# Optimization experiments

Measured on AMD Instinct MI355X. Metric: run time of the kernel, lower is better.

## Reference

```python
import jax, jax.numpy as jnp
import numpy as np

LOW_T = 25.5   # 0.1 * 255
HIGH_T = 76.5  # 0.3 * 255


def _dwconv3x3(img, k):
    # img: [B, C, H, W]; k: [3, 3]; depthwise conv with replicate border (as OpenCV Sobel)
    B, C, H, W = img.shape
    p = jnp.pad(img, ((0, 0), (0, 0), (1, 1), (1, 1)), mode='edge')
    kern = jnp.broadcast_to(k.astype(img.dtype), (C, 1, 3, 3))
    return jax.lax.conv_general_dilated(p, kern, (1, 1), 'VALID', feature_group_count=C)


def _shift(a, dy, dx):
    # a: [B, H, W]; shift by (dy, dx), zero at out-of-range borders
    B, H, W = a.shape
    p = jnp.pad(a, ((0, 0), (1, 1), (1, 1)))
    return p[:, 1 + dy:1 + dy + H, 1 + dx:1 + dx + W]


def canny(x, low, high):
    # x: [B, 3, H, W] in [0, 1]
    B, C, H, W = x.shape
    img = jnp.floor(jnp.clip(x, 0.0, 1.0) * 255.0)  # uint8 quantization, kept float

    kx = jnp.array([[-1., 0., 1.], [-2., 0., 2.], [-1., 0., 1.]])
    ky = jnp.array([[-1., -2., -1.], [0., 0., 0.], [1., 2., 1.]])
    gx = _dwconv3x3(img, kx)  # [B, C, H, W]
    gy = _dwconv3x3(img, ky)

    # L1 gradient magnitude (OpenCV default L2gradient=False); multi-channel:
    # pick the channel with max magnitude per pixel (OpenCV behavior)
    mag_c = jnp.abs(gx) + jnp.abs(gy)                      # [B, C, H, W]
    idx = jnp.argmax(mag_c, axis=1, keepdims=True)         # [B, 1, H, W]
    gxs = jnp.take_along_axis(gx, idx, axis=1)[:, 0]       # [B, H, W]
    gys = jnp.take_along_axis(gy, idx, axis=1)[:, 0]
    mag = jnp.take_along_axis(mag_c, idx, axis=1)[:, 0]

    # Non-maximum suppression: quantize gradient direction into 4 bins
    PI = np.float32(np.pi)
    ang = jnp.mod(jnp.arctan2(gys, gxs), PI)               # [0, pi)
    b = (jnp.floor((ang + PI / 8) / (PI / 4)).astype(jnp.int32)) % 4  # [B, H, W]

    # neighbor offsets along gradient direction per bin: 0deg, 45deg, 90deg, 135deg
    offs = [((0, 1), (0, -1)), ((1, 1), (-1, -1)), ((1, 0), (-1, 0)), ((1, -1), (-1, 1))]
    s1 = jnp.stack([_shift(mag, dy, dx) for (dy, dx), _ in offs])   # [4, B, H, W]
    s2 = jnp.stack([_shift(mag, dy, dx) for _, (dy, dx) in offs])
    n1 = jnp.take_along_axis(s1, b[None], axis=0)[0]
    n2 = jnp.take_along_axis(s2, b[None], axis=0)[0]
    nms = jnp.where((mag >= n1) & (mag >= n2), mag, 0.0)

    # Double threshold + hysteresis (8-connected propagation to fixed point)
    strong = (nms > high).astype(x.dtype)
    weak = (nms > low).astype(x.dtype)

    def cond(c):
        return c[1]

    def body(c):
        s, _ = c
        d = jax.lax.reduce_window(s, 0.0, jax.lax.max, (1, 3, 3), (1, 1, 1), 'SAME')
        ns = jnp.maximum(s, d * weak)
        return ns, jnp.any(ns != s)

    edges, _ = jax.lax.while_loop(cond, body, (strong, jnp.array(True)))

    # cv2.cvtColor GRAY2RGB then /255 -> {0, 1} replicated over 3 channels
    return jnp.broadcast_to(edges[:, None], (B, C, H, W))


def setup_inputs() -> dict:
    key = jax.random.key(0)
    x = jax.random.uniform(key, (16, 3, 720, 1280), dtype=jnp.float32)
    return {"x": x}


def reference(x):
    return canny(x, LOW_T, HIGH_T)
```

## Files before the change

### kernel.cpp

```cpp
#include <hip/hip_runtime.h>
#include <hip/hip_cooperative_groups.h>
#include <stdint.h>

namespace cg = cooperative_groups;
typedef unsigned long long u64;

static constexpr int BB  = 16;
static constexpr int HH  = 720;
static constexpr int WW  = 1280;
static constexpr int HWP = HH * WW;
static constexpr int WORDS_X = WW / 64;
static constexpr long long OUT_ELEMS = (long long)BB * 3 * HWP;
static constexpr size_t OUT_BYTES = (size_t)OUT_ELEMS * 4;
static constexpr size_t PLANE_B = (size_t)BB * HH * WORDS_X * 8;
static constexpr int N16 = (int)(OUT_ELEMS / 16);
static constexpr int KGRID = 512;
static constexpr int KNT = KGRID * 256;
static constexpr int OSLOT = (N16 + KNT - 1) / KNT;

typedef short v4s __attribute__((ext_vector_type(4)));
union QW { u64 u; v4s v; uint2 p; };

__device__ __forceinline__ int dirbin_b(int gx, int gy)
{
    int u  = (gy < 0) ? -gx : gx;
    int vv = gy < 0 ? -gy : gy;
    int A  = u < 0 ? -u : u;
    int b2 = 2 * A * A;
    int tt = vv + A;
    int dd = vv - A;
    bool P1 = (tt * tt < b2);
    bool P2 = (dd < 0) || (dd * dd < b2);
    return P1 ? 0 : (P2 ? ((u > 0) ? 1 : 3) : 2);
}

__global__ __launch_bounds__(256)
void k_gradnms(const float* __restrict__ x, u64* __restrict__ splane,
               u64* __restrict__ wplane)
{
    __shared__ __align__(16) u64 qimg[20][72];
    __shared__ int mtile[18][68];

    const int blk = blockIdx.x;
    const int bx = blk % 20;
    const int t1 = blk / 20;
    const int by = t1 % 45;
    const int b  = t1 / 45;
    const int x0 = bx << 6, y0 = by << 4;
    const float* bp = x + (size_t)b * 3 * HWP;

    for (int i = threadIdx.x; i < 20 * 34; i += 256) {
        int r   = i / 34;
        int pc  = i - r * 34;
        int col = pc * 2;
        int gy = y0 - 2 + r;   gy = gy < 0 ? 0 : (gy > HH - 1 ? HH - 1 : gy);
        int gx = x0 - 2 + col;
        const float* row = bp + (size_t)gy * WW;
        float a0, a1, b0, b1, c0, c1;
        if (gx >= 0 && gx + 1 < WW) {
            float2 fa = *(const float2*)(row + gx);
            float2 fb = *(const float2*)(row + HWP + gx);
            float2 fc = *(const float2*)(row + 2 * HWP + gx);
            a0 = fa.x; a1 = fa.y; b0 = fb.x; b1 = fb.y; c0 = fc.x; c1 = fc.y;
        } else {
            int g0 = gx     < 0 ? 0 : (gx     > WW - 1 ? WW - 1 : gx);
            int g1 = gx + 1 < 0 ? 0 : (gx + 1 > WW - 1 ? WW - 1 : gx + 1);
            a0 = row[g0];           a1 = row[g1];
            b0 = row[HWP + g0];     b1 = row[HWP + g1];
            c0 = row[2 * HWP + g0]; c1 = row[2 * HWP + g1];
        }
        uint32_t qa0 = (uint32_t)(fminf(fmaxf(a0, 0.f), 1.f) * 255.f);
        uint32_t qb0 = (uint32_t)(fminf(fmaxf(b0, 0.f), 1.f) * 255.f);
        uint32_t qc0 = (uint32_t)(fminf(fmaxf(c0, 0.f), 1.f) * 255.f);
        uint32_t qa1 = (uint32_t)(fminf(fmaxf(a1, 0.f), 1.f) * 255.f);
        uint32_t qb1 = (uint32_t)(fminf(fmaxf(b1, 0.f), 1.f) * 255.f);
        uint32_t qc1 = (uint32_t)(fminf(fmaxf(c1, 0.f), 1.f) * 255.f);
        ulonglong2 wv;
        wv.x = (u64)(qa0 | (qb0 << 16)) | ((u64)qc0 << 32);
        wv.y = (u64)(qa1 | (qb1 << 16)) | ((u64)qc1 << 32);
        *(ulonglong2*)&qimg[r][col] = wv;
    }
    __syncthreads();

    if (threadIdx.x < 18 * 14) {
        int r  = threadIdx.x / 14;
        int g  = threadIdx.x - r * 14;
        int c0 = g * 5;
        int my = y0 - 1 + r;
        bool rowok = (my >= 0 && my < HH);
        v4s s[7], t[7];
#pragma unroll
        for (int k = 0; k < 7; ++k) {
            QW w0, w1, w2;
            w0.u = qimg[r    ][c0 + k];
            w1.u = qimg[r + 1][c0 + k];
            w2.u = qimg[r + 2][c0 + k];
            s[k] = w0.v + w1.v + w1.v + w2.v;
            t[k] = w2.v - w0.v;
        }
        int mx0 = x0 - 1 + c0;
#pragma unroll
        for (int j = 0; j < 5; ++j) {
            int c = c0 + j;
            if (c >= 66) continue;
            int pk = 0;
            int mx = mx0 + j;
            if (rowok && mx >= 0 && mx < WW) {
                v4s gx4 = s[j + 2] - s[j];
                v4s gy4 = t[j] + t[j + 1] + t[j + 1] + t[j + 2];
                v4s ax = __builtin_elementwise_max(gx4, -gx4);
                v4s ay = __builtin_elementwise_max(gy4, -gy4);
                QW mq; mq.v = ax + ay;
                int m0 = (int)(mq.p.x & 0xffffu);
                int m1 = (int)(mq.p.x >> 16);
                int m2 = (int)(mq.p.y & 0xffffu);
                int bm = m0, bi = 0;
                if (m1 > bm) { bm = m1; bi = 1; }
                if (m2 > bm) { bm = m2; bi = 2; }
                QW gq; gq.v = gx4;
                QW hq; hq.v = gy4;
                uint32_t gw = (bi == 2) ? gq.p.y : gq.p.x;
                uint32_t hw = (bi == 2) ? hq.p.y : hq.p.x;
                int hi16 = (bi == 1) ? 16 : 0;
                int bgx = (int)(short)(gw >> hi16);
                int bgy = (int)(short)(hw >> hi16);
                pk = bm | (dirbin_b(bgx, bgy) << 12);
            }
            mtile[r][c] = pk;
        }
    }
    __syncthreads();

    const int v = threadIdx.x >> 6, l = threadIdx.x & 63;
#pragma unroll
    for (int k = 0; k < 4; ++k) {
        int ry = v * 4 + k;
        int pk = mtile[ry + 1][l + 1];
        int m = pk & 0xFFF, bin = pk >> 12;
        int dy = (bin == 0) ? 0 : 1;
        int dx = (bin == 2) ? 0 : ((bin == 3) ? -1 : 1);
        int n1 = mtile[ry + 1 + dy][l + 1 + dx] & 0xFFF;
        int n2 = mtile[ry + 1 - dy][l + 1 - dx] & 0xFFF;
        int keep = (m >= n1) && (m >= n2);
        u64 sB = __ballot(keep && m >= 77);
        u64 wB = __ballot(keep && m >= 26);
        if (l == 0) {
            size_t rb = ((size_t)b * HH + (y0 + ry)) * WORDS_X + bx;
            splane[rb] = sB;
            wplane[rb] = wB;
        }
    }
}

__device__ __forceinline__ u64 sh_up(u64 x, int k) {
    int l = threadIdx.x & 63;
    u64 y = __shfl(x, l - k, 64);
    return (l >= k) ? y : 0ull;
}
__device__ __forceinline__ u64 sh_dn(u64 x, int k) {
    int l = threadIdx.x & 63;
    u64 y = __shfl(x, l + k, 64);
    return (l + k < 64) ? y : 0ull;
}
__device__ __forceinline__ u64 dil(u64 x) { return x | (x << 1) | (x >> 1); }

__device__ __forceinline__ u64 hflood_L(u64 f, u64 w) {
    u64 p = w;
    f |= p & (f << 1);  p &= (p << 1);
    f |= p & (f << 2);  p &= (p << 2);
    f |= p & (f << 4);  p &= (p << 4);
    f |= p & (f << 8);  p &= (p << 8);
    f |= p & (f << 16); p &= (p << 16);
    f |= p & (f << 32);
    return f;
}
__device__ __forceinline__ u64 hflood_R(u64 f, u64 w) {
    u64 p = w;
    f |= p & (f >> 1);  p &= (p >> 1);
    f |= p & (f >> 2);  p &= (p >> 2);
    f |= p & (f >> 4);  p &= (p >> 4);
    f |= p & (f >> 8);  p &= (p >> 8);
    f |= p & (f >> 16); p &= (p >> 16);
    f |= p & (f >> 32);
    return f;
}

__global__ __launch_bounds__(768, 3)
void k_hyst_local(u64* __restrict__ splane, const u64* __restrict__ wplane)
{
    __shared__ u64 sTop[12][20], sBot[12][20];
    __shared__ int schg[2];

    const int b = blockIdx.x;
    const int r = threadIdx.x;
    const int l = threadIdx.x & 63;
    const int v = threadIdx.x >> 6;
    const bool valid = r < HH;
    const size_t base = ((size_t)b * HH + (valid ? r : 0)) * WORDS_X;

    u64 W[20], F[20];
#pragma unroll
    for (int j = 0; j < 20; ++j) {
        W[j] = valid ? wplane[base + j] : 0ull;
        F[j] = valid ? splane[base + j] : 0ull;
    }

    auto converge_band = [&]() {
        while (true) {
            u64 carry = 0;
#pragma unroll
            for (int j = 0; j < 20; ++j) {
                u64 f = F[j] | (W[j] & carry);
                f = hflood_L(f, W[j]);
                F[j] = f;
                carry = (f >> 63) & 1ull;
            }
            carry = 0;
#pragma unroll
            for (int j = 19; j >= 0; --j) {
                u64 f = F[j] | (W[j] & (carry << 63));
                f = hflood_R(f, W[j]);
                F[j] = f;
                carry = f & 1ull;
            }
            int ch = 0;
            u64 po = 0;
            u64 cur = F[0];
#pragma unroll
            for (int j = 0; j < 20; ++j) {
                u64 nx = (j < 19) ? F[j + 1] : 0ull;
                u64 n = dil(cur) | ((po >> 63) & 1ull) | ((nx & 1ull) << 63);
                po = cur; cur = nx;
                u64 add = W[j] & (sh_up(n, 1) | sh_dn(n, 1)) & ~F[j];
                ch |= (add != 0ull);
                F[j] |= add;
            }
            if (!__any(ch)) break;
        }
    };

    if (threadIdx.x == 0) { schg[0] = 0; schg[1] = 0; }
    converge_band();

    int iter = 0;
    while (true) {
        const int c = iter & 1;
        if (threadIdx.x == 0) schg[c ^ 1] = 0;

        if (l == 0 || l == 63) {
#pragma unroll
            for (int j = 0; j < 20; ++j) {
                u64 d = dil(F[j]);
                if (j > 0)  d |= (F[j-1] >> 63) & 1ull;
                if (j < 19) d |= (F[j+1] & 1ull) << 63;
                if (l == 0) sTop[v][j] = d; else sBot[v][j] = d;
            }
        }
        __syncthreads();

        int anynb = 0;
#pragma unroll
        for (int j = 0; j < 20; ++j) {
            u64 s = 0ull;
            if (l == 0  && v > 0)  s = sBot[v-1][j];
            else if (l == 63 && v < 11) s = sTop[v+1][j];
            u64 add = W[j] & s & ~F[j];
            anynb |= (add != 0ull);
            F[j] |= add;
        }
        if (__any(anynb)) {
            converge_band();
            schg[c] = 1;
        }
        __syncthreads();
        if (!schg[c]) break;
        ++iter;
    }

#pragma unroll
    for (int j = 0; j < 20; ++j)
        if (valid) splane[base + j] = F[j];
}

__global__ __launch_bounds__(256)
void k_out(const u64* __restrict__ splane, float* __restrict__ out)
{
    int i = blockIdx.x * 256 + threadIdx.x;
    int px  = i * 16;
    int bb  = px / (3 * HWP);
    int rem = px - bb * (3 * HWP);
    int yx  = rem % HWP;
    int y   = yx / WW;
    int xx  = yx - y * WW;
    u64 wv = splane[((size_t)bb * HH + y) * WORDS_X + (xx >> 6)];
    uint32_t bits = (uint32_t)((wv >> (xx & 63)) & 0xFFFFull);
    float4* o4 = (float4*)(out + (size_t)i * 16);
#pragma unroll
    for (int q = 0; q < 4; ++q) {
        float4 fv;
        fv.x = (bits >> (q * 4 + 0)) & 1 ? 1.0f : 0.0f;
        fv.y = (bits >> (q * 4 + 1)) & 1 ? 1.0f : 0.0f;
        fv.z = (bits >> (q * 4 + 2)) & 1 ? 1.0f : 0.0f;
        fv.w = (bits >> (q * 4 + 3)) & 1 ? 1.0f : 0.0f;
        o4[q] = fv;
    }
}

__global__ __launch_bounds__(256, 4)
void k_out_capture(const u64* __restrict__ splane, float* __restrict__ out)
{
    cg::grid_group grid = cg::this_grid();
    const int gtid = blockIdx.x * 256 + threadIdx.x;
    uint32_t vals[OSLOT];
#pragma unroll
    for (int n = 0; n < OSLOT; ++n) {
        int i = gtid + n * KNT;
        if (i < N16) {
            int px  = i * 16;
            int bb  = px / (3 * HWP);
            int rem = px - bb * (3 * HWP);
            int yx  = rem % HWP;
            int y   = yx / WW;
            int xx  = yx - y * WW;
            u64 wv = splane[((size_t)bb * HH + y) * WORDS_X + (xx >> 6)];
            vals[n] = (uint32_t)((wv >> (xx & 63)) & 0xFFFFull);
        }
    }
    grid.sync();
#pragma unroll
    for (int n = 0; n < OSLOT; ++n) {
        int i = gtid + n * KNT;
        if (i < N16) {
            uint32_t bits = vals[n];
            float4* o4 = (float4*)(out + (size_t)i * 16);
#pragma unroll
            for (int q = 0; q < 4; ++q) {
                float4 fv;
                fv.x = (bits >> (q * 4 + 0)) & 1 ? 1.0f : 0.0f;
                fv.y = (bits >> (q * 4 + 1)) & 1 ? 1.0f : 0.0f;
                fv.z = (bits >> (q * 4 + 2)) & 1 ? 1.0f : 0.0f;
                fv.w = (bits >> (q * 4 + 3)) & 1 ? 1.0f : 0.0f;
                o4[q] = fv;
            }
        }
    }
}

extern "C" void kernel_launch(void* const* d_in, const int* in_sizes, int n_in,
                              void* d_out, int out_size, void* d_ws, size_t ws_size,
                              hipStream_t stream)
{
    const float* x = (const float*)d_in[0];
    float* out = (float*)d_out;

    const bool use_ws = (d_ws != nullptr) && (ws_size >= 2 * PLANE_B);
    u64 *splane, *wplane;
    if (use_ws) {
        splane = (u64*)d_ws;
        wplane = (u64*)((char*)d_ws + PLANE_B);
    } else {
        char* tail = (char*)d_out + OUT_BYTES;
        wplane = (u64*)(tail - PLANE_B);
        splane = (u64*)(tail - 2 * PLANE_B);
    }

    k_gradnms<<<20 * 45 * BB, 256, 0, stream>>>(x, splane, wplane);
    k_hyst_local<<<BB, 768, 0, stream>>>(splane, wplane);

    if (use_ws) {
        k_out<<<N16 / 256, 256, 0, stream>>>(splane, out);
    } else {
        void* args[] = { (void*)&splane, (void*)&out };
        hipLaunchCooperativeKernel((void*)k_out_capture, dim3(KGRID), dim3(256),
                                   args, 0, stream);
    }
}
```

Baseline: 207.7 us.

## Use overlapping 64-row bands with halo rows in hysteresis kernel

Replaces the 12-wave band decomposition with 16 waves of 64 rows that overlap by 9 halo rows on each side, each wave owning 45 interior rows. Owned boundary rows are published to shared memory every outer iteration and copied into neighboring waves' halo rows. Because each wave also floods through its halos, fewer cross-band sync iterations should be needed. The cost is about 42% more threads doing redundant flood work, a large shared buffer and a 1024-thread block with only one block per CU.

New measurement: 232.8 us. +12.1%, slower.

```diff
diff --git a/kernel.cpp b/kernel.cpp
--- a/kernel.cpp
+++ b/kernel.cpp
@@ -17,6 +17,8 @@
 static constexpr int KGRID = 512;
 static constexpr int KNT = KGRID * 256;
 static constexpr int OSLOT = (N16 + KNT - 1) / KNT;
+static constexpr int HSTR = 45;
+static constexpr int PFS2 = 21;
 
 typedef short v4s __attribute__((ext_vector_type(4)));
 union QW { u64 u; v4s v; uint2 p; };
@@ -185,18 +187,20 @@
     return f;
 }
 
-__global__ __launch_bounds__(768, 3)
-void k_hyst_local(u64* __restrict__ splane, const u64* __restrict__ wplane)
-{
-    __shared__ u64 sTop[12][20], sBot[12][20];
+__global__ __launch_bounds__(1024, 1)
+void k_hyst_overlap(u64* __restrict__ splane, const u64* __restrict__ wplane)
+{
+    __shared__ u64 pf[HH * PFS2];
     __shared__ int schg[2];
 
     const int b = blockIdx.x;
-    const int r = threadIdx.x;
     const int l = threadIdx.x & 63;
     const int v = threadIdx.x >> 6;
-    const bool valid = r < HH;
-    const size_t base = ((size_t)b * HH + (valid ? r : 0)) * WORDS_X;
+    const int row = HSTR * v - 9 + l;
+    const bool valid = (row >= 0) && (row < HH);
+    const bool own   = valid && (l >= 9) && (l < 54);
+    const bool pub   = own && (l < 20 || l >= 43);
+    const size_t base = ((size_t)b * HH + (valid ? row : 0)) * WORDS_X;
 
     u64 W[20], F[20];
 #pragma unroll
@@ -245,30 +249,53 @@
     int iter = 0;
     while (true) {
         const int c = iter & 1;
+
+        if (pub) {
+#pragma unroll
+            for (int j = 0; j < 20; ++j) pf[row * PFS2 + j] = F[j];
+        }
         if (threadIdx.x == 0) schg[c ^ 1] = 0;
-
-        if (l == 0 || l == 63) {
+        __syncthreads();
+
+        int addf = 0;
+        if (valid && !own) {
 #pragma unroll
             for (int j = 0; j < 20; ++j) {
-                u64 d = dil(F[j]);
-                if (j > 0)  d |= (F[j-1] >> 63) & 1ull;
-                if (j < 19) d |= (F[j+1] & 1ull) << 63;
-                if (l == 0) sTop[v][j] = d; else sBot[v][j] = d;
-            }
-        }
-        __syncthreads();
-
-        int anynb = 0;
-#pragma unroll
-        for (int j = 0; j < 20; ++j) {
-            u64 s = 0ull;
-            if (l == 0  && v > 0)  s = sBot[v-1][j];
-            else if (l == 63 && v < 11) s = sTop[v+1][j];
-            u64 add = W[j] & s & ~F[j];
-            anynb |= (add != 0ull);
-            F[j] |= add;
-        }
-        if (__any(anynb)) {
+                u64 a = pf[row * PFS2 + j] & ~F[j];
+                addf |= (a != 0ull);
+                F[j] |= a;
+            }
+        }
+        if (l == 0 && row - 1 >= 0) {
+            u64 pr[20];
+#pragma unroll
+            for (int j = 0; j < 20; ++j) pr[j] = pf[(row - 1) * PFS2 + j];
+#pragma unroll
+            for (int j = 0; j < 20; ++j) {
+                u64 s = dil(pr[j]);
+                if (j > 0)  s |= (pr[j - 1] >> 63) & 1ull;
+                if (j < 19) s |= (pr[j + 1] & 1ull) << 63;
+                u64 a = W[j] & s & ~F[j];
+                addf |= (a != 0ull);
+                F[j] |= a;
+            }
+        }
+        if (l == 63 && valid && row + 1 < HH) {
+            u64 pr[20];
+#pragma unroll
+            for (int j = 0; j < 20; ++j) pr[j] = pf[(row + 1) * PFS2 + j];
+#pragma unroll
+            for (int j = 0; j < 20; ++j) {
+                u64 s = dil(pr[j]);
+                if (j > 0)  s |= (pr[j - 1] >> 63) & 1ull;
+                if (j < 19) s |= (pr[j + 1] & 1ull) << 63;
+                u64 a = W[j] & s & ~F[j];
+                addf |= (a != 0ull);
+                F[j] |= a;
+            }
+        }
+
+        if (__any(addf)) {
             converge_band();
             schg[c] = 1;
         }
@@ -279,7 +306,7 @@
 
 #pragma unroll
     for (int j = 0; j < 20; ++j)
-        if (valid) splane[base + j] = F[j];
+        if (own) splane[base + j] = F[j];
 }
 
 __global__ __launch_bounds__(256)
@@ -365,7 +392,7 @@
     }
 
     k_gradnms<<<20 * 45 * BB, 256, 0, stream>>>(x, splane, wplane);
-    k_hyst_local<<<BB, 768, 0, stream>>>(splane, wplane);
+    k_hyst_overlap<<<BB, 1024, 0, stream>>>(splane, wplane);
 
     if (use_ws) {
         k_out<<<N16 / 256, 256, 0, stream>>>(splane, out);
```
